# Performance work log

Hardware: AMD Instinct MI355X
Metric: run time of the kernel (lower is better)

Reference implementation:

```python
import jax, jax.numpy as jnp
import numpy as np

B, S, H = 2, 2048, 4096
NH, HD = 32, 128          # num attention heads, head dim (kv_channels)
KVH = 2                   # multi_query_group_num (KV heads)
ROT = HD // 2             # 64 rotary dims -> rope cache last-2 dim = 32
QKV = NH * HD + 2 * KVH * HD  # 4608


def apply_rope(x, rope):
    # x: [b, nh, s, hd]; rope: [b, s, ROT//2, 2]
    b, nh, s, hd = x.shape
    x_rot, x_pass = x[..., :ROT], x[..., ROT:]
    xs = x_rot.reshape(b, nh, s, ROT // 2, 2)
    rc = rope[:, :s].reshape(b, 1, s, ROT // 2, 2)
    out = jnp.stack([
        xs[..., 0] * rc[..., 0] - xs[..., 1] * rc[..., 1],
        xs[..., 1] * rc[..., 0] + xs[..., 0] * rc[..., 1],
    ], axis=-1).reshape(b, nh, s, ROT)
    return jnp.concatenate([out, x_pass], axis=-1)


def setup_inputs() -> dict:
    key = jax.random.key(0)
    ks = jax.random.split(key, 6)
    hidden_states = jax.random.normal(ks[0], (B, S, H), dtype=jnp.float32)
    rotary_pos_emb = jax.random.normal(ks[1], (B, S, ROT // 2, 2), dtype=jnp.float32)
    # causal mask: True = masked (strict upper triangle), matching module's ~tril
    causal = jnp.triu(jnp.ones((S, S), dtype=jnp.bool_), k=1)
    attention_mask = jnp.broadcast_to(causal[None, None], (B, 1, S, S))
    W_qkv = jax.random.normal(ks[2], (QKV, H), dtype=jnp.float32) * (1.0 / np.sqrt(H))
    b_qkv = jax.random.normal(ks[3], (QKV,), dtype=jnp.float32) * 0.02
    W_dense = jax.random.normal(ks[4], (H, NH * HD), dtype=jnp.float32) * (1.0 / np.sqrt(NH * HD))
    return {"hidden_states": hidden_states, "rotary_pos_emb": rotary_pos_emb,
            "attention_mask": attention_mask, "W_qkv": W_qkv, "b_qkv": b_qkv,
            "W_dense": W_dense}


def reference(hidden_states, rotary_pos_emb, attention_mask, W_qkv, b_qkv, W_dense):
    b, s, _ = hidden_states.shape
    mixed = hidden_states @ W_qkv.T + b_qkv  # [b, s, QKV]
    q, k, v = jnp.split(mixed, [NH * HD, NH * HD + KVH * HD], axis=-1)
    q = q.reshape(b, s, NH, HD).transpose(0, 2, 1, 3)   # [b, NH, s, hd]
    k = k.reshape(b, s, KVH, HD).transpose(0, 2, 1, 3)  # [b, KVH, s, hd]
    v = v.reshape(b, s, KVH, HD).transpose(0, 2, 1, 3)
    q = apply_rope(q, rotary_pos_emb)
    k = apply_rope(k, rotary_pos_emb)
    # GQA expand KV heads to NH
    rep = NH // KVH
    k = jnp.repeat(k, rep, axis=1)
    v = jnp.repeat(v, rep, axis=1)
    scale = 1.0 / np.sqrt(HD)
    scores = jnp.einsum('bhqd,bhkd->bhqk', q, k).astype(jnp.float32) * scale
    scores = jnp.where(attention_mask, -jnp.inf, scores)
    probs = jax.nn.softmax(scores, axis=-1).astype(v.dtype)
    ctx = jnp.einsum('bhqk,bhkd->bhqd', probs, v)       # [b, NH, s, hd]
    ctx = ctx.transpose(0, 2, 1, 3).reshape(b, s, NH * HD)
    return ctx @ W_dense.T
```

## Files before the change

### kernel.cpp

```cpp
#include <hip/hip_runtime.h>
#include <hip/hip_bf16.h>
#include <stdint.h>

#define Bb 2
#define Ss 2048
#define Hh 4096
#define NHh 32
#define HDd 128
#define KVHh 2

typedef __attribute__((ext_vector_type(8))) short bf16x8;
typedef __attribute__((ext_vector_type(4))) float f32x4;
typedef __attribute__((ext_vector_type(16))) float f32x16;
typedef __attribute__((ext_vector_type(4))) unsigned int u32x4;
typedef unsigned short u16;
typedef unsigned int u32;
typedef unsigned long long u64;

__device__ __forceinline__ u16 f2b(float f) {
  union { float f; u32 u; } v; v.f = f;
  u32 r = v.u + 0x7fffu + ((v.u >> 16) & 1u);
  return (u16)(r >> 16);
}
__device__ __forceinline__ float b2f(u16 h) {
  union { u32 u; float f; } v; v.u = ((u32)h) << 16;
  return v.f;
}

__device__ __forceinline__ u32 cvtpk(float lo, float hi_) {
  u32 r;
  asm("v_cvt_pk_bf16_f32 %0, %1, %2" : "=v"(r) : "v"(lo), "v"(hi_));
  return r;
}
__device__ __forceinline__ void plswap(u32& x, u32& y) {
  asm volatile("v_permlane32_swap_b32 %0, %1" : "+v"(x), "+v"(y));
}

__device__ __forceinline__ void gload_lds16(const u16* g, u16* l) {
  __builtin_amdgcn_global_load_lds(
      (const __attribute__((address_space(1))) u32*)(uintptr_t)g,
      (__attribute__((address_space(3))) u32*)(u32)(uintptr_t)l,
      16, 0, 0);
}

__global__ void cvt_k(const float* __restrict__ in, u16* __restrict__ out, int n) {
  int i = blockIdx.x * blockDim.x + threadIdx.x;
  int idx = i * 4;
  if (idx >= n) return;
  float4 v = *(const float4*)&in[idx];
  u64 pack = (u64)f2b(v.x) | ((u64)f2b(v.y) << 16) |
             ((u64)f2b(v.z) << 32) | ((u64)f2b(v.w) << 48);
  *(u64*)&out[idx] = pack;
}

__global__ void rope_k(u16* __restrict__ X, const float* __restrict__ rope, int nheads) {
  int i = blockIdx.x * blockDim.x + threadIdx.x;
  int p = i & 31;
  int s = (i >> 5) & (Ss - 1);
  int bh = i >> 16;
  if (bh >= Bb * nheads) return;
  int b = bh / nheads;
  size_t base = ((size_t)bh * Ss + s) * HDd + p * 2;
  u32 x01 = *(u32*)&X[base];
  float x0 = b2f((u16)(x01 & 0xffff));
  float x1 = b2f((u16)(x01 >> 16));
  float2 rc = *(const float2*)&rope[(((size_t)b * Ss + s) * 32 + p) * 2];
  float o0 = x0 * rc.x - x1 * rc.y;
  float o1 = x1 * rc.x + x0 * rc.y;
  u32 o = (u32)f2b(o0) | ((u32)f2b(o1) << 16);
  *(u32*)&X[base] = o;
}

template <int KK>
__device__ __forceinline__ void stage_tileA(const u16* __restrict__ gbase, u16* dst, int tid) {
#pragma unroll
  for (int li = 0; li < 2; ++li) {
    int t16 = li * 512 + tid;
    int rt = t16 >> 2, ct = t16 & 3;
    int cg = ct ^ ((rt >> 1) & 3);
    gload_lds16(gbase + (size_t)rt * KK + cg * 8, dst + t16 * 8);
  }
}
template <int KK>
__device__ __forceinline__ void stage_tileB(const u16* __restrict__ gbase, u16* dst, int tid) {
  int t16 = tid;
  int rt = t16 >> 2, ct = t16 & 3;
  int cg = ct ^ ((rt >> 1) & 3);
  gload_lds16(gbase + (size_t)rt * KK + cg * 8, dst + t16 * 8);
}

__device__ __forceinline__ bf16x8 frag128(const u16* buf, int row, int lk) {
  int ch = lk ^ ((row >> 1) & 3);
  return *(const bf16x8*)&buf[row * 32 + ch * 8];
}

template <int NN, int KK, int COLG, int EPI>
__global__ __launch_bounds__(512, 4) void gemm256x128(
    const u16* __restrict__ A, const u16* __restrict__ Bm,
    float* __restrict__ Cout, const float* __restrict__ bias,
    u16* __restrict__ Qb, u16* __restrict__ Kb, u16* __restrict__ Vb) {
  __shared__ u16 As[2][8192];
  __shared__ u16 Bs[2][4096];
  const int tid = threadIdx.x;
  const int wave = tid >> 6;
  const int lane = tid & 63;
  const int lr = lane & 15;
  const int lk = lane >> 4;
  const int wr = wave >> 1;
  const int wc = wave & 1;
  const int bid = blockIdx.x;
  const int xcd = bid & 7;
  const int local = bid >> 3;
  const int rlr = local / COLG;
  const int rlc = local - rlr * COLG;
  const int m0 = ((xcd >> 2) * 8 + rlr) * 256;
  const int n0 = ((xcd & 3) * COLG + rlc) * 128;
  const int NT = KK / 32;

  f32x4 acc[4][4];
#pragma unroll
  for (int i = 0; i < 4; ++i)
#pragma unroll
    for (int j = 0; j < 4; ++j) acc[i][j] = (f32x4){0.f, 0.f, 0.f, 0.f};

  const u16* Ab = A + (size_t)m0 * KK;
  const u16* Bb_ = Bm + (size_t)n0 * KK;

  stage_tileA<KK>(Ab, &As[0][0], tid);
  stage_tileB<KK>(Bb_, &Bs[0][0], tid);
  asm volatile("s_waitcnt vmcnt(0)");
  __syncthreads();

  int cur = 0;
  for (int t = 0; t < NT; ++t) {
    if (t + 1 < NT) {
      stage_tileA<KK>(Ab + (t + 1) * 32, &As[cur ^ 1][0], tid);
      stage_tileB<KK>(Bb_ + (t + 1) * 32, &Bs[cur ^ 1][0], tid);
      asm volatile("s_waitcnt vmcnt(3)");
    } else {
      asm volatile("s_waitcnt vmcnt(0)");
    }
    __builtin_amdgcn_s_barrier();
    __builtin_amdgcn_sched_barrier(0);

    bf16x8 af[4], bf[4];
#pragma unroll
    for (int mi = 0; mi < 4; ++mi)
      af[mi] = frag128(&As[cur][0], wr * 64 + mi * 16 + lr, lk);
#pragma unroll
    for (int ni = 0; ni < 4; ++ni)
      bf[ni] = frag128(&Bs[cur][0], wc * 64 + ni * 16 + lr, lk);
    asm volatile("s_waitcnt lgkmcnt(0)");
    __builtin_amdgcn_sched_barrier(0);
    __builtin_amdgcn_s_setprio(1);
#pragma unroll
    for (int mi = 0; mi < 4; ++mi)
#pragma unroll
      for (int ni = 0; ni < 4; ++ni)
        acc[mi][ni] = __builtin_amdgcn_mfma_f32_16x16x32_bf16(af[mi], bf[ni], acc[mi][ni], 0, 0, 0);
    __builtin_amdgcn_s_setprio(0);
    __builtin_amdgcn_s_barrier();
    cur ^= 1;
  }

  if constexpr (EPI == 0) {
#pragma unroll
    for (int mi = 0; mi < 4; ++mi)
#pragma unroll
      for (int ni = 0; ni < 4; ++ni) {
        int col = n0 + wc * 64 + ni * 16 + lr;
        int rowb = m0 + wr * 64 + mi * 16 + lk * 4;
#pragma unroll
        for (int j = 0; j < 4; ++j)
          Cout[(size_t)(rowb + j) * NN + col] = acc[mi][ni][j];
      }
  } else {
#pragma unroll
    for (int ni = 0; ni < 4; ++ni) {
      int n = n0 + wc * 64 + ni * 16 + lr;
      float bv = bias[n];
#pragma unroll
      for (int mi = 0; mi < 4; ++mi) {
        int mb = m0 + wr * 64 + mi * 16 + lk * 4;
#pragma unroll
        for (int j = 0; j < 4; ++j) {
          int m = mb + j;
          int bb = m >> 11;
          int ss = m & 2047;
          u16 hv = f2b(acc[mi][ni][j] + bv);
          if (n < 4096) {
            Qb[(((size_t)bb * NHh + (n >> 7)) * Ss + ss) * HDd + (n & 127)] = hv;
          } else if (n < 4352) {
            int idx2 = n - 4096;
            Kb[(((size_t)bb * KVHh + (idx2 >> 7)) * Ss + ss) * HDd + (idx2 & 127)] = hv;
          } else {
            int idx2 = n - 4352;
            Vb[(((size_t)bb * KVHh + (idx2 >> 7)) * Ss + ss) * HDd + (idx2 & 127)] = hv;
          }
        }
      }
    }
  }
}

__global__ __launch_bounds__(512, 2) void attn_k(
    const u16* __restrict__ Qb, const u16* __restrict__ Kb,
    const u16* __restrict__ Vb, u16* __restrict__ Ctx) {
  __shared__ u16 Kt[2][64 * 128];
  __shared__ u16 Vt[2][128 * 64];
  const int tid = threadIdx.x;
  const int w = tid >> 6;
  const int lane = tid & 63;
  const int l31 = lane & 31;
  const int hi = lane >> 5;
  const int h = blockIdx.y, b = blockIdx.z;
  const int hkv = h >> 4;
  const u16* Qp = Qb + ((size_t)(b * NHh + h)) * Ss * HDd;
  const u16* Kp = Kb + ((size_t)(b * KVHh + hkv)) * Ss * HDd;
  const u16* Vp = Vb + ((size_t)(b * KVHh + hkv)) * Ss * HDd;

  const float scale = 0.08838834764831845f;
  const float L2E = 1.4426950408889634f;

  for (int hp = 0; hp < 2; ++hp) {
    const int qt = hp == 0 ? (7 - (int)blockIdx.x) : (int)blockIdx.x;
    const int qs = qt * 256;
    const int qw = qs + w * 32;
    const int qrow = qw + l31;
    const int nt = qs / 64 + 4;

    bf16x8 qf[8];
#pragma unroll
    for (int ds = 0; ds < 8; ++ds)
      qf[ds] = *(const bf16x8*)&Qp[(size_t)qrow * HDd + ds * 16 + hi * 8];

    f32x16 accO[4];
#pragma unroll
    for (int i = 0; i < 4; ++i)
#pragma unroll
      for (int r = 0; r < 16; ++r) accO[i][r] = 0.f;
    float m_r = -3.0e38f, l_r = 0.f;

    {
#pragma unroll
      for (int i = 0; i < 2; ++i) {
        int slot = w * 2 + i;
        int r = slot * 4 + (lane >> 4);
        int p = lane & 15;
        int gc = (p & 8) | ((p ^ r) & 7);
        gload_lds16(Kp + (size_t)r * HDd + gc * 8, &Kt[0][slot * 512]);
      }
      bf16x8 v0 = *(const bf16x8*)&Vp[(size_t)lane * HDd + w * 16];
      bf16x8 v1 = *(const bf16x8*)&Vp[(size_t)lane * HDd + w * 16 + 8];
      u32x4 sv = __builtin_bit_cast(u32x4, (lane & 1) ? v0 : v1);
      u32x4 rv;
      rv.x = __shfl_xor(sv.x, 1); rv.y = __shfl_xor(sv.y, 1);
      rv.z = __shfl_xor(sv.z, 1); rv.w = __shfl_xor(sv.w, 1);
      bf16x8 recv = __builtin_bit_cast(bf16x8, rv);
      int kvp = lane >> 1;
#pragma unroll
      for (int i = 0; i < 8; ++i) {
        int d = w * 16 + (lane & 1) * 8 + i;
        u16 lo = (lane & 1) ? (u16)recv[i] : (u16)v0[i];
        u16 hb = (lane & 1) ? (u16)v1[i] : (u16)recv[i];
        u32 val = (u32)lo | ((u32)hb << 16);
        int cp = (kvp >> 2) ^ (d & 7);
        *(u32*)&Vt[0][d * 64 + cp * 8 + (kvp & 3) * 2] = val;
      }
    }
    __syncthreads();

    for (int t = 0; t < nt; ++t) {
      const int j0 = t * 64;
      const int cur = t & 1;
      const bool havenext = (t + 1 < nt);
      bf16x8 nv0, nv1;
      if (havenext) {
        const int j1 = j0 + 64;
#pragma unroll
        for (int i = 0; i < 2; ++i) {
          int slot = w * 2 + i;
          int r = slot * 4 + (lane >> 4);
          int p = lane & 15;
          int gc = (p & 8) | ((p ^ r) & 7);
          gload_lds16(Kp + (size_t)(j1 + r) * HDd + gc * 8, &Kt[cur ^ 1][slot * 512]);
        }
        nv0 = *(const bf16x8*)&Vp[(size_t)(j1 + lane) * HDd + w * 16];
        nv1 = *(const bf16x8*)&Vp[(size_t)(j1 + lane) * HDd + w * 16 + 8];
      }

      if (j0 <= qw + 31) {
        f32x16 aS[2];
#pragma unroll
        for (int a = 0; a < 2; ++a)
#pragma unroll
          for (int r = 0; r < 16; ++r) aS[a][r] = 0.f;
#pragma unroll
        for (int kvb = 0; kvb < 2; ++kvb) {
          int r = kvb * 32 + l31;
#pragma unroll
          for (int ds = 0; ds < 8; ++ds) {
            int c = ds * 2 + hi;
            int cp = (c & 8) | ((c ^ r) & 7);
            bf16x8 kf = *(const bf16x8*)&Kt[cur][r * 128 + cp * 8];
            aS[kvb] = __builtin_amdgcn_mfma_f32_32x32x16_bf16(kf, qf[ds], aS[kvb], 0, 0, 0);
          }
        }
        const bool needmask = (j0 + 63 > qw);
        float mx = -3.0e38f;
#pragma unroll
        for (int a = 0; a < 2; ++a)
#pragma unroll
          for (int r = 0; r < 16; ++r) {
            float s = aS[a][r] * scale;
            if (needmask) {
              int kv = j0 + a * 32 + (r & 3) + 8 * (r >> 2) + 4 * hi;
              s = (kv > qrow) ? -3.0e38f : s;
            }
            aS[a][r] = s;
            mx = fmaxf(mx, s);
          }
        mx = fmaxf(mx, __shfl_xor(mx, 32));
        float mnew = fmaxf(m_r, mx);
        float corr = __builtin_amdgcn_exp2f((m_r - mnew) * L2E);
        float sum = 0.f;
#pragma unroll
        for (int a = 0; a < 2; ++a)
#pragma unroll
          for (int r = 0; r < 16; ++r) {
            float pe = __builtin_amdgcn_exp2f((aS[a][r] - mnew) * L2E);
            aS[a][r] = pe;
            sum += pe;
          }
        sum += __shfl_xor(sum, 32);
        l_r = l_r * corr + sum;
        m_r = mnew;
#pragma unroll
        for (int i = 0; i < 4; ++i)
#pragma unroll
          for (int r = 0; r < 16; ++r) accO[i][r] *= corr;

        u32 cc0[2][4], cc1[2][4];
#pragma unroll
        for (int a = 0; a < 2; ++a)
#pragma unroll
          for (int g = 0; g < 4; ++g) {
            cc0[a][g] = cvtpk(aS[a][g * 4 + 0], aS[a][g * 4 + 1]);
            cc1[a][g] = cvtpk(aS[a][g * 4 + 2], aS[a][g * 4 + 3]);
          }
        bf16x8 pa[4];
#pragma unroll
        for (int ks = 0; ks < 4; ++ks) {
          int a = ks >> 1, g0 = (ks & 1) * 2;
          u32 w0 = cc0[a][g0], w2 = cc0[a][g0 + 1];
          u32 w1 = cc1[a][g0], w3 = cc1[a][g0 + 1];
          plswap(w0, w2);
          plswap(w1, w3);
          u32x4 tv; tv.x = w0; tv.y = w1; tv.z = w2; tv.w = w3;
          pa[ks] = __builtin_bit_cast(bf16x8, tv);
        }
#pragma unroll
        for (int dblk = 0; dblk < 4; ++dblk) {
          int d = dblk * 32 + l31;
#pragma unroll
          for (int ks = 0; ks < 4; ++ks) {
            int c = ks * 2 + hi;
            int cp = c ^ (d & 7);
            bf16x8 vf = *(const bf16x8*)&Vt[cur][d * 64 + cp * 8];
            accO[dblk] = __builtin_amdgcn_mfma_f32_32x32x16_bf16(vf, pa[ks], accO[dblk], 0, 0, 0);
          }
        }
      }

      if (havenext) {
        u32x4 sv = __builtin_bit_cast(u32x4, (lane & 1) ? nv0 : nv1);
        u32x4 rv;
        rv.x = __shfl_xor(sv.x, 1); rv.y = __shfl_xor(sv.y, 1);
        rv.z = __shfl_xor(sv.z, 1); rv.w = __shfl_xor(sv.w, 1);
        bf16x8 recv = __builtin_bit_cast(bf16x8, rv);
        int kvp = lane >> 1;
#pragma unroll
        for (int i = 0; i < 8; ++i) {
          int d = w * 16 + (lane & 1) * 8 + i;
          u16 lo = (lane & 1) ? (u16)recv[i] : (u16)nv0[i];
          u16 hb = (lane & 1) ? (u16)nv1[i] : (u16)recv[i];
          u32 val = (u32)lo | ((u32)hb << 16);
          int cp = (kvp >> 2) ^ (d & 7);
          *(u32*)&Vt[cur ^ 1][d * 64 + cp * 8 + (kvp & 3) * 2] = val;
        }
      }
      __syncthreads();
    }

    {
      float il = 1.0f / l_r;
      size_t rb = ((size_t)b * Ss + qrow) * (size_t)(NHh * HDd) + (size_t)h * HDd;
#pragma unroll
      for (int dblk = 0; dblk < 4; ++dblk)
#pragma unroll
        for (int g = 0; g < 4; ++g) {
          int d0 = dblk * 32 + g * 8 + hi * 4;
          u64 pack = (u64)f2b(accO[dblk][g * 4 + 0] * il) |
                     ((u64)f2b(accO[dblk][g * 4 + 1] * il) << 16) |
                     ((u64)f2b(accO[dblk][g * 4 + 2] * il) << 32) |
                     ((u64)f2b(accO[dblk][g * 4 + 3] * il) << 48);
          *(u64*)&Ctx[rb + d0] = pack;
        }
    }
    __syncthreads();
  }
}

extern "C" void kernel_launch(void* const* d_in, const int* in_sizes, int n_in,
                              void* d_out, int out_size, void* d_ws, size_t ws_size,
                              hipStream_t stream) {
  const float* hidden = (const float*)d_in[0];
  const float* rope = (const float*)d_in[1];
  const float* Wqkv = (const float*)d_in[3];
  const float* bqkv = (const float*)d_in[4];
  const float* Wdense = (const float*)d_in[5];
  float* out = (float*)d_out;

  char* w = (char*)d_ws;
  u16* Xbf = (u16*)w;
  u16* ctx = Xbf;
  w += (size_t)33554432;
  u16* Wq = (u16*)w;
  u16* Wd = Wq;
  w += (size_t)37748736;
  u16* Qb = (u16*)w; w += (size_t)33554432;
  u16* Kb = (u16*)w; w += (size_t)2097152;
  u16* Vb = (u16*)w; w += (size_t)2097152;

  cvt_k<<<(16777216 / 4 + 255) / 256, 256, 0, stream>>>(hidden, Xbf, 16777216);
  cvt_k<<<(18874368 / 4 + 255) / 256, 256, 0, stream>>>(Wqkv, Wq, 18874368);
  gemm256x128<4608, 4096, 9, 1><<<dim3(576), 512, 0, stream>>>(
      Xbf, Wq, nullptr, bqkv, Qb, Kb, Vb);
  rope_k<<<(Bb * NHh * Ss * 32 + 255) / 256, 256, 0, stream>>>(Qb, rope, NHh);
  rope_k<<<(Bb * KVHh * Ss * 32 + 255) / 256, 256, 0, stream>>>(Kb, rope, KVHh);
  cvt_k<<<(16777216 / 4 + 255) / 256, 256, 0, stream>>>(Wdense, Wd, 16777216);
  attn_k<<<dim3(4, NHh, Bb), 512, 0, stream>>>(Qb, Kb, Vb, ctx);
  gemm256x128<4096, 4096, 8, 0><<<dim3(512), 512, 0, stream>>>(
      ctx, Wd, out, nullptr, nullptr, nullptr, nullptr);
}
```

Before: 510.9 us.

## Fuse Q RoPE into attention, merge conversions, and add lazy softmax rescaling

Applies rotary embedding to Q fragments inside the attention kernel after loading, removing the separate Q rope pass over the Q buffer. Merges the hidden and QKV-weight fp32-to-bf16 conversions into one launch. Skips the online-softmax max update and accumulator rescale unless the new tile max exceeds the running max by more than a threshold, saving VALU work per tile. The lazy rescale lets unnormalised probabilities exceed one, slightly affecting bf16 precision.

```diff
diff --git a/kernel.cpp b/kernel.cpp
--- a/kernel.cpp
+++ b/kernel.cpp
@@ -43,10 +43,24 @@
       16, 0, 0);
 }
 
-__global__ void cvt_k(const float* __restrict__ in, u16* __restrict__ out, int n) {
+__global__ void cvt2_k(const float* __restrict__ a, u16* __restrict__ oa,
+                       const float* __restrict__ b, u16* __restrict__ ob) {
+  int i = blockIdx.x * blockDim.x + threadIdx.x;
+  const float* src;
+  u16* dst;
+  int off;
+  if (i < 4194304) { src = a; dst = oa; off = i; }
+  else { src = b; dst = ob; off = i - 4194304; }
+  int idx = off * 4;
+  float4 v = *(const float4*)&src[idx];
+  u64 pack = (u64)f2b(v.x) | ((u64)f2b(v.y) << 16) |
+             ((u64)f2b(v.z) << 32) | ((u64)f2b(v.w) << 48);
+  *(u64*)&dst[idx] = pack;
+}
+
+__global__ void cvtW_k(const float* __restrict__ in, u16* __restrict__ out) {
   int i = blockIdx.x * blockDim.x + threadIdx.x;
   int idx = i * 4;
-  if (idx >= n) return;
   float4 v = *(const float4*)&in[idx];
   u64 pack = (u64)f2b(v.x) | ((u64)f2b(v.y) << 16) |
              ((u64)f2b(v.z) << 32) | ((u64)f2b(v.w) << 48);
@@ -205,7 +219,8 @@
 
 __global__ __launch_bounds__(512, 2) void attn_k(
     const u16* __restrict__ Qb, const u16* __restrict__ Kb,
-    const u16* __restrict__ Vb, u16* __restrict__ Ctx) {
+    const u16* __restrict__ Vb, const float* __restrict__ rope,
+    u16* __restrict__ Ctx) {
   __shared__ u16 Kt[2][64 * 128];
   __shared__ u16 Vt[2][128 * 64];
   const int tid = threadIdx.x;
@@ -233,6 +248,20 @@
 #pragma unroll
     for (int ds = 0; ds < 8; ++ds)
       qf[ds] = *(const bf16x8*)&Qp[(size_t)qrow * HDd + ds * 16 + hi * 8];
+#pragma unroll
+    for (int ds = 0; ds < 4; ++ds) {
+      bf16x8 q = qf[ds];
+      bf16x8 o;
+#pragma unroll
+      for (int i = 0; i < 4; ++i) {
+        int p = ds * 8 + hi * 4 + i;
+        float2 rc = *(const float2*)&rope[(((size_t)b * Ss + qrow) * 32 + p) * 2];
+        float x0 = b2f((u16)q[2 * i]), x1 = b2f((u16)q[2 * i + 1]);
+        o[2 * i] = (short)f2b(x0 * rc.x - x1 * rc.y);
+        o[2 * i + 1] = (short)f2b(x1 * rc.x + x0 * rc.y);
+      }
+      qf[ds] = o;
+    }
 
     f32x16 accO[4];
 #pragma unroll
@@ -321,24 +350,27 @@
             mx = fmaxf(mx, s);
           }
         mx = fmaxf(mx, __shfl_xor(mx, 32));
-        float mnew = fmaxf(m_r, mx);
-        float corr = __builtin_amdgcn_exp2f((m_r - mnew) * L2E);
+        if (!__all(mx - m_r <= 8.0f)) {
+          float mnew = fmaxf(m_r, mx);
+          float corr = __builtin_amdgcn_exp2f((m_r - mnew) * L2E);
+          l_r *= corr;
+#pragma unroll
+          for (int i = 0; i < 4; ++i)
+#pragma unroll
+            for (int r = 0; r < 16; ++r) accO[i][r] *= corr;
+          m_r = mnew;
+        }
         float sum = 0.f;
 #pragma unroll
         for (int a = 0; a < 2; ++a)
 #pragma unroll
           for (int r = 0; r < 16; ++r) {
-            float pe = __builtin_amdgcn_exp2f((aS[a][r] - mnew) * L2E);
+            float pe = __builtin_amdgcn_exp2f((aS[a][r] - m_r) * L2E);
             aS[a][r] = pe;
             sum += pe;
           }
         sum += __shfl_xor(sum, 32);
-        l_r = l_r * corr + sum;
-        m_r = mnew;
-#pragma unroll
-        for (int i = 0; i < 4; ++i)
-#pragma unroll
-          for (int r = 0; r < 16; ++r) accO[i][r] *= corr;
+        l_r += sum;
 
         u32 cc0[2][4], cc1[2][4];
 #pragma unroll
@@ -432,14 +464,12 @@
   u16* Kb = (u16*)w; w += (size_t)2097152;
   u16* Vb = (u16*)w; w += (size_t)2097152;
 
-  cvt_k<<<(16777216 / 4 + 255) / 256, 256, 0, stream>>>(hidden, Xbf, 16777216);
-  cvt_k<<<(18874368 / 4 + 255) / 256, 256, 0, stream>>>(Wqkv, Wq, 18874368);
+  cvt2_k<<<34816, 256, 0, stream>>>(hidden, Xbf, Wqkv, Wq);
   gemm256x128<4608, 4096, 9, 1><<<dim3(576), 512, 0, stream>>>(
       Xbf, Wq, nullptr, bqkv, Qb, Kb, Vb);
-  rope_k<<<(Bb * NHh * Ss * 32 + 255) / 256, 256, 0, stream>>>(Qb, rope, NHh);
   rope_k<<<(Bb * KVHh * Ss * 32 + 255) / 256, 256, 0, stream>>>(Kb, rope, KVHh);
-  cvt_k<<<(16777216 / 4 + 255) / 256, 256, 0, stream>>>(Wdense, Wd, 16777216);
-  attn_k<<<dim3(4, NHh, Bb), 512, 0, stream>>>(Qb, Kb, Vb, ctx);
+  cvtW_k<<<16384, 256, 0, stream>>>(Wdense, Wd);
+  attn_k<<<dim3(4, NHh, Bb), 512, 0, stream>>>(Qb, Kb, Vb, rope, ctx);
   gemm256x128<4096, 4096, 8, 0><<<dim3(512), 512, 0, stream>>>(
       ctx, Wd, out, nullptr, nullptr, nullptr, nullptr);
 }
```

Measured after the change: 490.5 us. -4.0%, faster.
